# Performance work log

Measured on AMD Instinct MI355X. Metric: run time of the kernel, lower is better.

Reference implementation:

```python
import jax, jax.numpy as jnp
import numpy as np

B, N, D_MODEL, H, LIN_K = 4, 4096, 1024, 16, 256
D_K = D_MODEL // H


def setup_inputs() -> dict:
    key = jax.random.key(0)
    ks = jax.random.split(key, 9)
    s = 1.0 / np.sqrt(D_MODEL)
    return {
        "K": jax.random.normal(ks[0], (B, N, D_MODEL), jnp.float32),
        "Q": jax.random.normal(ks[1], (B, N, D_MODEL), jnp.float32),
        "V": jax.random.normal(ks[2], (B, N, D_MODEL), jnp.float32),
        "We": jax.random.normal(ks[3], (N, LIN_K), jnp.float32) / np.sqrt(N),
        "be": jnp.zeros((LIN_K,), jnp.float32),
        "Wf": jax.random.normal(ks[4], (N, LIN_K), jnp.float32) / np.sqrt(N),
        "bf": jnp.zeros((LIN_K,), jnp.float32),
        "Wo": jax.random.normal(ks[5], (D_MODEL, D_MODEL), jnp.float32) * s,
        "bo": jnp.zeros((D_MODEL,), jnp.float32),
        "n_heads": H,
    }


def reference(K, Q, V, We, be, Wf, bf, Wo, bo, n_heads):
    b, n, d_model = K.shape
    d_k = d_model // n_heads
    split = lambda x: x.reshape(b, n, n_heads, d_k).transpose(0, 2, 1, 3)  # [b,h,n,d]
    Kh, Qh, Vh = split(K), split(Q), split(V)
    # Linformer projection: Dense(k) applied to K^T [b,h,d,n] -> [b,h,d,k]
    Kp = jnp.einsum("bhnd,nk->bhdk", Kh, We) + be
    scores = jnp.einsum("bhnd,bhdk->bhnk", Qh, Kp) / jnp.sqrt(jnp.float32(d_k))
    P = jax.nn.softmax(scores, axis=-1)  # dropout rate 0.0 -> identity
    # V projection: Dense(k) on V^T then transpose back -> [b,h,k,d]
    Vp = jnp.einsum("bhnd,nk->bhkd", Vh, Wf) + bf[:, None]
    out = jnp.einsum("bhnk,bhkd->bhnd", P, Vp)
    out = out.transpose(0, 2, 1, 3).reshape(b, n, d_model)
    return out @ Wo + bo
```

## Files before the change

kernel.cpp:

```cpp
#include <hip/hip_runtime.h>
#include <hip/hip_bf16.h>

#define BB      4
#define SEQ     4096
#define DMODEL  1024
#define NHEAD   16
#define DK      64
#define LK      256
#define BH      (BB*NHEAD)

typedef unsigned short u16;
typedef unsigned int   u32;
typedef float f32x4  __attribute__((ext_vector_type(4)));
typedef _Float16 f16x8 __attribute__((ext_vector_type(8)));

__device__ __forceinline__ u16 f2h(float f) {
    _Float16 h = (_Float16)f;
    u16 r; __builtin_memcpy(&r, &h, 2); return r;
}
__device__ __forceinline__ u32 packh(float a, float b) {
    return (u32)f2h(a) | ((u32)f2h(b) << 16);
}
__device__ __forceinline__ void gl2lds16(const void* g, void* l) {
    __builtin_amdgcn_global_load_lds(
        (const __attribute__((address_space(1))) unsigned int*)g,
        (__attribute__((address_space(3))) unsigned int*)l,
        16, 0, 0);
}

__global__ __launch_bounds__(256) void tconv(
    const float* __restrict__ src, u16* __restrict__ dst,
    int ss, int ds, size_t sbo, size_t dbo)
{
    const float* S = src + (size_t)blockIdx.z * sbo;
    u16* D         = dst + (size_t)blockIdx.z * dbo;
    const int r0 = blockIdx.x * 64;
    const int c0 = blockIdx.y * 64;
    __shared__ float T[64][65];
    const int t = threadIdx.x;
    {
        int rr = (t >> 4) * 4;
        int cc = (t & 15) * 4;
#pragma unroll
        for (int i = 0; i < 4; ++i) {
            float4 v = *(const float4*)(S + (size_t)(r0 + rr + i) * ss + c0 + cc);
            T[rr + i][cc + 0] = v.x; T[rr + i][cc + 1] = v.y;
            T[rr + i][cc + 2] = v.z; T[rr + i][cc + 3] = v.w;
        }
    }
    __syncthreads();
    int cr = t >> 2, rc = (t & 3) * 16;
    u32 o[8];
#pragma unroll
    for (int j = 0; j < 8; ++j)
        o[j] = packh(T[rc + 2 * j][cr], T[rc + 2 * j + 1][cr]);
    u16* d = D + (size_t)(c0 + cr) * ds + r0 + rc;
    *(uint4*)(d)     = make_uint4(o[0], o[1], o[2], o[3]);
    *(uint4*)(d + 8) = make_uint4(o[4], o[5], o[6], o[7]);
}

__global__ __launch_bounds__(256) void wo_convert(
    const float* __restrict__ Wo, u16* __restrict__ WoT)
{
    const int n0 = blockIdx.x * 64, k0 = blockIdx.y * 64;
    __shared__ float T[64][65];
    const int t = threadIdx.x;
    {
        int kr = (t >> 4) * 4;
        int nc = (t & 15) * 4;
#pragma unroll
        for (int i = 0; i < 4; ++i) {
            float4 v = *(const float4*)(Wo + (size_t)(k0 + kr + i) * DMODEL + n0 + nc);
            T[kr + i][nc + 0] = v.x; T[kr + i][nc + 1] = v.y;
            T[kr + i][nc + 2] = v.z; T[kr + i][nc + 3] = v.w;
        }
    }
    __syncthreads();
    int n = t >> 2, kc = (t & 3) * 16;
    u32 o[8];
#pragma unroll
    for (int j = 0; j < 8; ++j)
        o[j] = packh(T[kc + j * 2][n], T[kc + j * 2 + 1][n]);
    u16* dst = WoT + (size_t)(n0 + n) * DMODEL + k0 + kc;
    *(uint4*)(dst)     = make_uint4(o[0], o[1], o[2], o[3]);
    *(uint4*)(dst + 8) = make_uint4(o[4], o[5], o[6], o[7]);
}

#define PROJ_BODY(Ab, Bb, bias, Cb, bias_on_row, c_row_stride, c0, r0)          \
    const int t  = threadIdx.x;                                                 \
    const int lane = t & 63;                                                    \
    const int w  = t >> 6;                                                      \
    const int wr = w >> 1, wc = w & 1;                                          \
    const int q  = lane >> 4, c = lane & 15;                                    \
    __shared__ u16 As[2][128 * 64];                                             \
    __shared__ u16 Bs[2][128 * 64];                                             \
    auto stage = [&](int buf, int kk) {                                         \
        _Pragma("unroll")                                                       \
        for (int i = 0; i < 4; ++i) {                                           \
            int li  = i * 256 + t;                                              \
            int row = li >> 3;                                                  \
            int c8  = (li & 7) ^ (row & 7);                                     \
            gl2lds16(Ab + (size_t)(r0 + row) * SEQ + kk + c8 * 8, &As[buf][(size_t)li * 8]); \
            gl2lds16(Bb + (size_t)(c0 + row) * SEQ + kk + c8 * 8, &Bs[buf][(size_t)li * 8]); \
        }                                                                       \
    };                                                                          \
    f32x4 acc[4][4];                                                            \
    _Pragma("unroll")                                                           \
    for (int m = 0; m < 4; ++m)                                                 \
        _Pragma("unroll")                                                       \
        for (int n = 0; n < 4; ++n) acc[m][n] = (f32x4){0.f, 0.f, 0.f, 0.f};    \
    stage(0, 0);                                                                \
    __syncthreads();                                                            \
    int cur = 0;                                                                \
    for (int k0 = 0; k0 < SEQ; k0 += 64) {                                      \
        if (k0 + 64 < SEQ) stage(cur ^ 1, k0 + 64);                             \
        _Pragma("unroll")                                                       \
        for (int s = 0; s < 2; ++s) {                                           \
            f16x8 af[4], bf[4];                                                 \
            _Pragma("unroll")                                                   \
            for (int m = 0; m < 4; ++m) {                                       \
                int row = wr * 64 + m * 16 + c;                                 \
                int c8  = (s * 4 + q) ^ (row & 7);                              \
                af[m] = *(const f16x8*)&As[cur][row * 64 + c8 * 8];             \
            }                                                                   \
            _Pragma("unroll")                                                   \
            for (int n = 0; n < 4; ++n) {                                       \
                int row = wc * 64 + n * 16 + c;                                 \
                int c8  = (s * 4 + q) ^ (row & 7);                              \
                bf[n] = *(const f16x8*)&Bs[cur][row * 64 + c8 * 8];             \
            }                                                                   \
            _Pragma("unroll")                                                   \
            for (int m = 0; m < 4; ++m)                                         \
                _Pragma("unroll")                                               \
                for (int n = 0; n < 4; ++n)                                     \
                    acc[m][n] = __builtin_amdgcn_mfma_f32_16x16x32_f16(af[m], bf[n], acc[m][n], 0, 0, 0); \
        }                                                                       \
        __syncthreads();                                                        \
        cur ^= 1;                                                               \
    }                                                                           \
    if (bias_on_row) {                                                          \
        _Pragma("unroll")                                                       \
        for (int m = 0; m < 4; ++m) {                                           \
            int rowb = r0 + wr * 64 + m * 16 + q * 4;                           \
            _Pragma("unroll")                                                   \
            for (int r = 0; r < 4; ++r) {                                       \
                float bv = bias[rowb + r];                                      \
                u16* dst = Cb + (size_t)(rowb + r) * c_row_stride + c0 + wc * 64 + c; \
                _Pragma("unroll")                                               \
                for (int n = 0; n < 4; ++n) dst[n * 16] = f2h(acc[m][n][r] + bv); \
            }                                                                   \
        }                                                                       \
    } else {                                                                    \
        float bv[4];                                                            \
        _Pragma("unroll")                                                       \
        for (int n = 0; n < 4; ++n) bv[n] = bias[c0 + wc * 64 + n * 16 + c];    \
        _Pragma("unroll")                                                       \
        for (int m = 0; m < 4; ++m) {                                           \
            int rowb = r0 + wr * 64 + m * 16 + q * 4;                           \
            _Pragma("unroll")                                                   \
            for (int r = 0; r < 4; ++r) {                                       \
                u16* dst = Cb + (size_t)(rowb + r) * c_row_stride + c0 + wc * 64 + c; \
                _Pragma("unroll")                                               \
                for (int n = 0; n < 4; ++n) dst[n * 16] = f2h(acc[m][n][r] + bv[n]); \
            }                                                                   \
        }                                                                       \
    }

__global__ __launch_bounds__(256) void proj_gemm(
    const u16* __restrict__ A, const u16* __restrict__ B,
    const float* __restrict__ bias, u16* __restrict__ Cout,
    int bias_on_row, size_t a_batch, size_t b_batch,
    int c_row_stride, size_t c_batch)
{
    const u16* Ab = A + (size_t)blockIdx.z * a_batch;
    const u16* Bb = B + (size_t)blockIdx.z * b_batch;
    u16* Cb       = Cout + (size_t)blockIdx.z * c_batch;
    const int c0 = blockIdx.x * 128;
    const int r0 = blockIdx.y * 128;
    PROJ_BODY(Ab, Bb, bias, Cb, bias_on_row, c_row_stride, c0, r0)
}

__global__ __launch_bounds__(256) void proj_both(
    const u16* __restrict__ WeT, const u16* __restrict__ WfT,
    const u16* __restrict__ KT,  const u16* __restrict__ VT,
    const float* __restrict__ be, const float* __restrict__ bfp,
    u16* __restrict__ KpF, u16* __restrict__ VpF)
{
    const int id = blockIdx.x;
    const u16 *Ab, *Bb; const float* bias; u16* Cb;
    int bias_on_row, c_row_stride, c0, r0;
    if (id < 64) {
        int b = id >> 4, s = id & 15;
        c0 = (s & 7) * 128; r0 = (s >> 3) * 128;
        Ab = WeT; Bb = KT + (size_t)b * DMODEL * SEQ;
        bias = be; bias_on_row = 1;
        Cb = KpF + (size_t)b * LK * DMODEL; c_row_stride = DMODEL;
    } else {
        int j = id - 64, b = j >> 4, s = j & 15;
        c0 = (s & 1) * 128; r0 = (s >> 1) * 128;
        Ab = VT + (size_t)b * DMODEL * SEQ; Bb = WfT;
        bias = bfp; bias_on_row = 0;
        Cb = VpF + (size_t)b * DMODEL * LK; c_row_stride = LK;
    }
    PROJ_BODY(Ab, Bb, bias, Cb, bias_on_row, c_row_stride, c0, r0)
}

__global__ __launch_bounds__(256) void attn_mfma(
    const float* __restrict__ Qin, const u16* __restrict__ KpF,
    const u16* __restrict__ VpF,   u16* __restrict__ AO)
{
    const int bh = blockIdx.y, b = bh >> 4, h = bh & 15;
    const int n0 = blockIdx.x * 64;
    const int t  = threadIdx.x;
    const int w    = t >> 6;
    const int lane = t & 63;
    const int q    = lane >> 4;
    const int c    = lane & 15;

    __shared__ u16 QO[64][72];
    __shared__ u16 KP[16896];
    __shared__ u16 Vl[16384];

    const u16* kbase = KpF + (size_t)b * LK * DMODEL + h * DK;
#pragma unroll
    for (int i = 0; i < 8; ++i) {
        int li = i * 256 + t;
        int row = li >> 3, ch = li & 7;
        int chs = ch ^ (row & 7);
        gl2lds16(kbase + (size_t)row * DMODEL + chs * 8, KP + (size_t)li * 8);
    }
    const u16* vbase = VpF + ((size_t)b * DMODEL + h * DK) * LK;
#pragma unroll
    for (int i = 0; i < 8; ++i) {
        int li = i * 256 + t;
        int row = li >> 5, ch = li & 31;
        int chs = (ch & 24) | ((ch & 7) ^ (row & 7));
        gl2lds16(vbase + (size_t)row * LK + chs * 8, Vl + (size_t)li * 8);
    }
    {
        int lr = lane >> 2, col0 = (lane & 3) * 16;
        const float* src = Qin + ((size_t)b * SEQ + n0 + w * 16 + lr) * DMODEL + h * DK + col0;
        float4 f0 = ((const float4*)src)[0];
        float4 f1 = ((const float4*)src)[1];
        float4 f2 = ((const float4*)src)[2];
        float4 f3 = ((const float4*)src)[3];
        uint4 p0, p1;
        p0.x = packh(f0.x, f0.y); p0.y = packh(f0.z, f0.w);
        p0.z = packh(f1.x, f1.y); p0.w = packh(f1.z, f1.w);
        p1.x = packh(f2.x, f2.y); p1.y = packh(f2.z, f2.w);
        p1.z = packh(f3.x, f3.y); p1.w = packh(f3.z, f3.w);
        *(uint4*)&QO[w * 16 + lr][col0]     = p0;
        *(uint4*)&QO[w * 16 + lr][col0 + 8] = p1;
    }
    __syncthreads();

    f16x8 a0 = *(const f16x8*)&QO[w * 16 + c][q * 8];
    f16x8 a1 = *(const f16x8*)&QO[w * 16 + c][32 + q * 8];

    f32x4 sc[16];
#pragma unroll
    for (int nt = 0; nt < 16; ++nt) sc[nt] = (f32x4){0.f, 0.f, 0.f, 0.f};
#pragma unroll
    for (int nt = 0; nt < 16; ++nt) {
        int ra = (nt * 16 + c) * 64;
        f16x8 b0 = *(const f16x8*)&KP[ra + ((q ^ (c & 7)) * 8)];
        f16x8 b1 = *(const f16x8*)&KP[ra + (((4 + q) ^ (c & 7)) * 8)];
        sc[nt] = __builtin_amdgcn_mfma_f32_16x16x32_f16(a0, b0, sc[nt], 0, 0, 0);
        sc[nt] = __builtin_amdgcn_mfma_f32_16x16x32_f16(a1, b1, sc[nt], 0, 0, 0);
    }

    float mx[4] = {-1e30f, -1e30f, -1e30f, -1e30f};
#pragma unroll
    for (int nt = 0; nt < 16; ++nt) {
        sc[nt] *= 0.125f;
#pragma unroll
        for (int r = 0; r < 4; ++r) mx[r] = fmaxf(mx[r], sc[nt][r]);
    }
#pragma unroll
    for (int d = 1; d < 16; d <<= 1)
#pragma unroll
        for (int r = 0; r < 4; ++r) mx[r] = fmaxf(mx[r], __shfl_xor(mx[r], d, 64));

    float sm[4] = {0.f, 0.f, 0.f, 0.f};
#pragma unroll
    for (int nt = 0; nt < 16; ++nt)
#pragma unroll
        for (int r = 0; r < 4; ++r) {
            float e = __expf(sc[nt][r] - mx[r]);
            sc[nt][r] = e;
            sm[r] += e;
        }
#pragma unroll
    for (int d = 1; d < 16; d <<= 1)
#pragma unroll
        for (int r = 0; r < 4; ++r) sm[r] += __shfl_xor(sm[r], d, 64);
    float inv[4];
#pragma unroll
    for (int r = 0; r < 4; ++r) inv[r] = 1.0f / sm[r];

    __syncthreads();

#pragma unroll
    for (int nt = 0; nt < 16; ++nt)
#pragma unroll
        for (int r = 0; r < 4; ++r)
            KP[(w * 16 + q * 4 + r) * 264 + nt * 16 + c] = f2h(sc[nt][r] * inv[r]);

    f32x4 ov[4];
#pragma unroll
    for (int nt = 0; nt < 4; ++nt) ov[nt] = (f32x4){0.f, 0.f, 0.f, 0.f};
#pragma unroll
    for (int ks = 0; ks < 8; ++ks) {
        f16x8 pa = *(const f16x8*)&KP[(w * 16 + c) * 264 + ks * 32 + q * 8];
#pragma unroll
        for (int nt = 0; nt < 4; ++nt) {
            int chunk = ks * 4 + q;
            int chs = (chunk & 24) | ((chunk & 7) ^ (c & 7));
            f16x8 vf = *(const f16x8*)&Vl[(nt * 16 + c) * 256 + chs * 8];
            ov[nt] = __builtin_amdgcn_mfma_f32_16x16x32_f16(pa, vf, ov[nt], 0, 0, 0);
        }
    }

#pragma unroll
    for (int nt = 0; nt < 4; ++nt)
#pragma unroll
        for (int r = 0; r < 4; ++r)
            QO[w * 16 + q * 4 + r][nt * 16 + c] = f2h(ov[nt][r]);

#pragma unroll
    for (int pass = 0; pass < 2; ++pass) {
        int lr  = w * 16 + pass * 8 + (lane >> 3);
        int col = (lane & 7) * 8;
        uint4 vv = *(uint4*)&QO[lr][col];
        *(uint4*)(AO + ((size_t)b * SEQ + n0 + lr) * DMODEL + h * DK + col) = vv;
    }
}

#define OBM 128
#define OBN 128
#define OBK 64

__global__ __launch_bounds__(256) void out_gemm_mfma(
    const u16* __restrict__ AO, const u16* __restrict__ WoT,
    const float* __restrict__ bo, float* __restrict__ Out)
{
    const int c0 = blockIdx.x * OBN;
    const int r0 = blockIdx.y * OBM;
    const int t  = threadIdx.x;
    const int lane = t & 63;
    const int w  = t >> 6;
    const int wr = w >> 1, wc = w & 1;
    const int q  = lane >> 4, c = lane & 15;

    __shared__ u16 As[OBM * OBK];
    __shared__ u16 Bs[OBN * OBK];

    f32x4 acc[4][4];
#pragma unroll
    for (int m = 0; m < 4; ++m)
#pragma unroll
        for (int n = 0; n < 4; ++n) acc[m][n] = (f32x4){0.f, 0.f, 0.f, 0.f};

    for (int k0 = 0; k0 < DMODEL; k0 += OBK) {
#pragma unroll
        for (int i = 0; i < 4; ++i) {
            int li  = i * 256 + t;
            int row = li >> 3;
            int c8  = (li & 7) ^ (row & 7);
            gl2lds16(AO  + (size_t)(r0 + row) * DMODEL + k0 + c8 * 8, (u16*)As + (size_t)li * 8);
            gl2lds16(WoT + (size_t)(c0 + row) * DMODEL + k0 + c8 * 8, (u16*)Bs + (size_t)li * 8);
        }
        __syncthreads();

#pragma unroll
        for (int s = 0; s < 2; ++s) {
            f16x8 af[4], bf[4];
#pragma unroll
            for (int m = 0; m < 4; ++m) {
                int row = wr * 64 + m * 16 + c;
                int c8  = (s * 4 + q) ^ (row & 7);
                af[m] = *(const f16x8*)&As[row * 64 + c8 * 8];
            }
#pragma unroll
            for (int n = 0; n < 4; ++n) {
                int row = wc * 64 + n * 16 + c;
                int c8  = (s * 4 + q) ^ (row & 7);
                bf[n] = *(const f16x8*)&Bs[row * 64 + c8 * 8];
            }
#pragma unroll
            for (int m = 0; m < 4; ++m)
#pragma unroll
                for (int n = 0; n < 4; ++n)
                    acc[m][n] = __builtin_amdgcn_mfma_f32_16x16x32_f16(af[m], bf[n], acc[m][n], 0, 0, 0);
        }
        __syncthreads();
    }

    float bv[4];
#pragma unroll
    for (int n = 0; n < 4; ++n) bv[n] = bo[c0 + wc * 64 + n * 16 + c];
#pragma unroll
    for (int m = 0; m < 4; ++m) {
        int rowb = r0 + wr * 64 + m * 16 + q * 4;
#pragma unroll
        for (int r = 0; r < 4; ++r) {
            float* dst = Out + (size_t)(rowb + r) * DMODEL + c0 + wc * 64 + c;
#pragma unroll
            for (int n = 0; n < 4; ++n) dst[n * 16] = acc[m][n][r] + bv[n];
        }
    }
}

extern "C" void kernel_launch(void* const* d_in, const int* in_sizes, int n_in,
                              void* d_out, int out_size, void* d_ws, size_t ws_size,
                              hipStream_t stream)
{
    const float* K   = (const float*)d_in[0];
    const float* Q   = (const float*)d_in[1];
    const float* V   = (const float*)d_in[2];
    const float* We  = (const float*)d_in[3];
    const float* be  = (const float*)d_in[4];
    const float* Wf  = (const float*)d_in[5];
    const float* bfp = (const float*)d_in[6];
    const float* Wo  = (const float*)d_in[7];
    const float* bo  = (const float*)d_in[8];
    float* Out = (float*)d_out;

    const size_t M1 = 1048576;
    const size_t TB = (size_t)BB * DMODEL * SEQ;

    if (ws_size >= 2 * (4 * M1 + 2 * TB)) {
        u16* KpF = (u16*)d_ws;
        u16* VpF = KpF + M1;
        u16* WeT = VpF + M1;
        u16* WfT = WeT + M1;
        u16* KT  = WfT + M1;
        u16* VT  = KT + TB;
        u16* AO  = KT;
        u16* WoT = WeT;

        tconv<<<dim3(SEQ / 64, LK / 64, 1), 256, 0, stream>>>(We, WeT, LK, SEQ, 0, 0);
        tconv<<<dim3(SEQ / 64, LK / 64, 1), 256, 0, stream>>>(Wf, WfT, LK, SEQ, 0, 0);
        tconv<<<dim3(SEQ / 64, DMODEL / 64, BB), 256, 0, stream>>>(
            K, KT, DMODEL, SEQ, (size_t)SEQ * DMODEL, (size_t)DMODEL * SEQ);
        tconv<<<dim3(SEQ / 64, DMODEL / 64, BB), 256, 0, stream>>>(
            V, VT, DMODEL, SEQ, (size_t)SEQ * DMODEL, (size_t)DMODEL * SEQ);
        proj_both<<<dim3(128), 256, 0, stream>>>(WeT, WfT, KT, VT, be, bfp, KpF, VpF);
        wo_convert<<<dim3(DMODEL / 64, DMODEL / 64), 256, 0, stream>>>(Wo, WoT);
        attn_mfma<<<dim3(SEQ / 64, BH), 256, 0, stream>>>(Q, KpF, VpF, AO);
        out_gemm_mfma<<<dim3(DMODEL / OBN, (BB * SEQ) / OBM), 256, 0, stream>>>(AO, WoT, bo, Out);
    } else {
        u16* KpF = (u16*)d_ws;
        u16* VpF = KpF + (size_t)BB * LK * DMODEL;
        u16* BIG = VpF + (size_t)BB * DMODEL * LK;
        u16* Wsm = BIG + (size_t)BB * SEQ * DMODEL;

        tconv<<<dim3(SEQ / 64, LK / 64, 1), 256, 0, stream>>>(We, Wsm, LK, SEQ, 0, 0);
        tconv<<<dim3(SEQ / 64, DMODEL / 64, BB), 256, 0, stream>>>(
            K, BIG, DMODEL, SEQ, (size_t)SEQ * DMODEL, (size_t)DMODEL * SEQ);
        proj_gemm<<<dim3(DMODEL / 128, LK / 128, BB), 256, 0, stream>>>(
            Wsm, BIG, be, KpF, 1, (size_t)0, (size_t)DMODEL * SEQ, DMODEL, (size_t)LK * DMODEL);
        tconv<<<dim3(SEQ / 64, LK / 64, 1), 256, 0, stream>>>(Wf, Wsm, LK, SEQ, 0, 0);
        tconv<<<dim3(SEQ / 64, DMODEL / 64, BB), 256, 0, stream>>>(
            V, BIG, DMODEL, SEQ, (size_t)SEQ * DMODEL, (size_t)DMODEL * SEQ);
        proj_gemm<<<dim3(LK / 128, DMODEL / 128, BB), 256, 0, stream>>>(
            BIG, Wsm, bfp, VpF, 0, (size_t)DMODEL * SEQ, (size_t)0, LK, (size_t)DMODEL * LK);
        wo_convert<<<dim3(DMODEL / 64, DMODEL / 64), 256, 0, stream>>>(Wo, Wsm);
        attn_mfma<<<dim3(SEQ / 64, BH), 256, 0, stream>>>(Q, KpF, VpF, BIG);
        out_gemm_mfma<<<dim3(DMODEL / OBN, (BB * SEQ) / OBM), 256, 0, stream>>>(BIG, Wsm, bo, Out);
    }
}
```

Before: 395.5 us.

## Make attention blocks persistent over 1024 rows to reuse projected K/V tiles

The attention kernel now uses 512-thread blocks that each handle 1024 query rows in 8 passes of 128. The projected K and V tiles for a head are loaded into LDS once per block instead of once per 64 rows. Q is read straight from global memory into registers and prefetched one pass ahead, with no LDS staging. The grid shrinks to 256 blocks, which lowers parallelism and latency hiding. The softmax probabilities and the output staging share one per-wave LDS region, relying on each wave's rows being private.

```diff
diff --git a/kernel.cpp b/kernel.cpp
--- a/kernel.cpp
+++ b/kernel.cpp
@@ -20,6 +20,12 @@
 }
 __device__ __forceinline__ u32 packh(float a, float b) {
     return (u32)f2h(a) | ((u32)f2h(b) << 16);
+}
+__device__ __forceinline__ f16x8 pack8h(float4 a, float4 b) {
+    union { uint4 u; f16x8 h; } r;
+    r.u = make_uint4(packh(a.x, a.y), packh(a.z, a.w),
+                     packh(b.x, b.y), packh(b.z, b.w));
+    return r.h;
 }
 __device__ __forceinline__ void gl2lds16(const void* g, void* l) {
     __builtin_amdgcn_global_load_lds(
@@ -205,134 +211,129 @@
     PROJ_BODY(Ab, Bb, bias, Cb, bias_on_row, c_row_stride, c0, r0)
 }
 
-__global__ __launch_bounds__(256) void attn_mfma(
+__global__ __launch_bounds__(512) void attn_mfma(
     const float* __restrict__ Qin, const u16* __restrict__ KpF,
     const u16* __restrict__ VpF,   u16* __restrict__ AO)
 {
     const int bh = blockIdx.y, b = bh >> 4, h = bh & 15;
-    const int n0 = blockIdx.x * 64;
+    const int n0 = blockIdx.x * 1024;
     const int t  = threadIdx.x;
     const int w    = t >> 6;
     const int lane = t & 63;
     const int q    = lane >> 4;
     const int c    = lane & 15;
 
-    __shared__ u16 QO[64][72];
-    __shared__ u16 KP[16896];
+    __shared__ u16 Kl[16384];
     __shared__ u16 Vl[16384];
+    __shared__ u16 Pl[128 * 264];
 
     const u16* kbase = KpF + (size_t)b * LK * DMODEL + h * DK;
 #pragma unroll
-    for (int i = 0; i < 8; ++i) {
-        int li = i * 256 + t;
+    for (int i = 0; i < 4; ++i) {
+        int li = i * 512 + t;
         int row = li >> 3, ch = li & 7;
         int chs = ch ^ (row & 7);
-        gl2lds16(kbase + (size_t)row * DMODEL + chs * 8, KP + (size_t)li * 8);
+        gl2lds16(kbase + (size_t)row * DMODEL + chs * 8, Kl + (size_t)li * 8);
     }
     const u16* vbase = VpF + ((size_t)b * DMODEL + h * DK) * LK;
 #pragma unroll
-    for (int i = 0; i < 8; ++i) {
-        int li = i * 256 + t;
+    for (int i = 0; i < 4; ++i) {
+        int li = i * 512 + t;
         int row = li >> 5, ch = li & 31;
         int chs = (ch & 24) | ((ch & 7) ^ (row & 7));
         gl2lds16(vbase + (size_t)row * LK + chs * 8, Vl + (size_t)li * 8);
     }
-    {
-        int lr = lane >> 2, col0 = (lane & 3) * 16;
-        const float* src = Qin + ((size_t)b * SEQ + n0 + w * 16 + lr) * DMODEL + h * DK + col0;
-        float4 f0 = ((const float4*)src)[0];
-        float4 f1 = ((const float4*)src)[1];
-        float4 f2 = ((const float4*)src)[2];
-        float4 f3 = ((const float4*)src)[3];
-        uint4 p0, p1;
-        p0.x = packh(f0.x, f0.y); p0.y = packh(f0.z, f0.w);
-        p0.z = packh(f1.x, f1.y); p0.w = packh(f1.z, f1.w);
-        p1.x = packh(f2.x, f2.y); p1.y = packh(f2.z, f2.w);
-        p1.z = packh(f3.x, f3.y); p1.w = packh(f3.z, f3.w);
-        *(uint4*)&QO[w * 16 + lr][col0]     = p0;
-        *(uint4*)&QO[w * 16 + lr][col0 + 8] = p1;
-    }
     __syncthreads();
 
-    f16x8 a0 = *(const f16x8*)&QO[w * 16 + c][q * 8];
-    f16x8 a1 = *(const f16x8*)&QO[w * 16 + c][32 + q * 8];
-
-    f32x4 sc[16];
-#pragma unroll
-    for (int nt = 0; nt < 16; ++nt) sc[nt] = (f32x4){0.f, 0.f, 0.f, 0.f};
-#pragma unroll
-    for (int nt = 0; nt < 16; ++nt) {
-        int ra = (nt * 16 + c) * 64;
-        f16x8 b0 = *(const f16x8*)&KP[ra + ((q ^ (c & 7)) * 8)];
-        f16x8 b1 = *(const f16x8*)&KP[ra + (((4 + q) ^ (c & 7)) * 8)];
-        sc[nt] = __builtin_amdgcn_mfma_f32_16x16x32_f16(a0, b0, sc[nt], 0, 0, 0);
-        sc[nt] = __builtin_amdgcn_mfma_f32_16x16x32_f16(a1, b1, sc[nt], 0, 0, 0);
-    }
-
-    float mx[4] = {-1e30f, -1e30f, -1e30f, -1e30f};
-#pragma unroll
-    for (int nt = 0; nt < 16; ++nt) {
-        sc[nt] *= 0.125f;
-#pragma unroll
-        for (int r = 0; r < 4; ++r) mx[r] = fmaxf(mx[r], sc[nt][r]);
-    }
-#pragma unroll
-    for (int d = 1; d < 16; d <<= 1)
-#pragma unroll
-        for (int r = 0; r < 4; ++r) mx[r] = fmaxf(mx[r], __shfl_xor(mx[r], d, 64));
-
-    float sm[4] = {0.f, 0.f, 0.f, 0.f};
-#pragma unroll
-    for (int nt = 0; nt < 16; ++nt)
-#pragma unroll
-        for (int r = 0; r < 4; ++r) {
-            float e = __expf(sc[nt][r] - mx[r]);
-            sc[nt][r] = e;
-            sm[r] += e;
-        }
-#pragma unroll
-    for (int d = 1; d < 16; d <<= 1)
-#pragma unroll
-        for (int r = 0; r < 4; ++r) sm[r] += __shfl_xor(sm[r], d, 64);
-    float inv[4];
-#pragma unroll
-    for (int r = 0; r < 4; ++r) inv[r] = 1.0f / sm[r];
-
-    __syncthreads();
-
-#pragma unroll
-    for (int nt = 0; nt < 16; ++nt)
-#pragma unroll
-        for (int r = 0; r < 4; ++r)
-            KP[(w * 16 + q * 4 + r) * 264 + nt * 16 + c] = f2h(sc[nt][r] * inv[r]);
-
-    f32x4 ov[4];
-#pragma unroll
-    for (int nt = 0; nt < 4; ++nt) ov[nt] = (f32x4){0.f, 0.f, 0.f, 0.f};
-#pragma unroll
-    for (int ks = 0; ks < 8; ++ks) {
-        f16x8 pa = *(const f16x8*)&KP[(w * 16 + c) * 264 + ks * 32 + q * 8];
-#pragma unroll
-        for (int nt = 0; nt < 4; ++nt) {
-            int chunk = ks * 4 + q;
-            int chs = (chunk & 24) | ((chunk & 7) ^ (c & 7));
-            f16x8 vf = *(const f16x8*)&Vl[(nt * 16 + c) * 256 + chs * 8];
-            ov[nt] = __builtin_amdgcn_mfma_f32_16x16x32_f16(pa, vf, ov[nt], 0, 0, 0);
-        }
-    }
-
-#pragma unroll
-    for (int nt = 0; nt < 4; ++nt)
-#pragma unroll
-        for (int r = 0; r < 4; ++r)
-            QO[w * 16 + q * 4 + r][nt * 16 + c] = f2h(ov[nt][r]);
-
-#pragma unroll
-    for (int pass = 0; pass < 2; ++pass) {
-        int lr  = w * 16 + pass * 8 + (lane >> 3);
-        int col = (lane & 7) * 8;
-        uint4 vv = *(uint4*)&QO[lr][col];
-        *(uint4*)(AO + ((size_t)b * SEQ + n0 + lr) * DMODEL + h * DK + col) = vv;
+    const float* qbase = Qin + ((size_t)b * SEQ + n0 + w * 16 + c) * DMODEL + h * DK;
+    const float4* qp0 = (const float4*)qbase;
+    float4 q0 = qp0[2 * q], q1 = qp0[2 * q + 1];
+    float4 q2 = qp0[8 + 2 * q], q3 = qp0[8 + 2 * q + 1];
+
+    for (int p = 0; p < 8; ++p) {
+        f16x8 a0 = pack8h(q0, q1);
+        f16x8 a1 = pack8h(q2, q3);
+        if (p < 7) {
+            const float4* qp = (const float4*)(qbase + (size_t)(p + 1) * 128 * DMODEL);
+            q0 = qp[2 * q]; q1 = qp[2 * q + 1];
+            q2 = qp[8 + 2 * q]; q3 = qp[8 + 2 * q + 1];
+        }
+
+        f32x4 sc[16];
+#pragma unroll
+        for (int nt = 0; nt < 16; ++nt) sc[nt] = (f32x4){0.f, 0.f, 0.f, 0.f};
+#pragma unroll
+        for (int nt = 0; nt < 16; ++nt) {
+            int ra = (nt * 16 + c) * 64;
+            f16x8 b0 = *(const f16x8*)&Kl[ra + ((q ^ (c & 7)) * 8)];
+            f16x8 b1 = *(const f16x8*)&Kl[ra + (((4 + q) ^ (c & 7)) * 8)];
+            sc[nt] = __builtin_amdgcn_mfma_f32_16x16x32_f16(a0, b0, sc[nt], 0, 0, 0);
+            sc[nt] = __builtin_amdgcn_mfma_f32_16x16x32_f16(a1, b1, sc[nt], 0, 0, 0);
+        }
+
+        float mx[4] = {-1e30f, -1e30f, -1e30f, -1e30f};
+#pragma unroll
+        for (int nt = 0; nt < 16; ++nt) {
+            sc[nt] *= 0.125f;
+#pragma unroll
+            for (int r = 0; r < 4; ++r) mx[r] = fmaxf(mx[r], sc[nt][r]);
+        }
+#pragma unroll
+        for (int d = 1; d < 16; d <<= 1)
+#pragma unroll
+            for (int r = 0; r < 4; ++r) mx[r] = fmaxf(mx[r], __shfl_xor(mx[r], d, 64));
+
+        float sm[4] = {0.f, 0.f, 0.f, 0.f};
+#pragma unroll
+        for (int nt = 0; nt < 16; ++nt)
+#pragma unroll
+            for (int r = 0; r < 4; ++r) {
+                float e = __expf(sc[nt][r] - mx[r]);
+                sc[nt][r] = e;
+                sm[r] += e;
+            }
+#pragma unroll
+        for (int d = 1; d < 16; d <<= 1)
+#pragma unroll
+            for (int r = 0; r < 4; ++r) sm[r] += __shfl_xor(sm[r], d, 64);
+        float inv[4];
+#pragma unroll
+        for (int r = 0; r < 4; ++r) inv[r] = 1.0f / sm[r];
+
+#pragma unroll
+        for (int nt = 0; nt < 16; ++nt)
+#pragma unroll
+            for (int r = 0; r < 4; ++r)
+                Pl[(w * 16 + q * 4 + r) * 264 + nt * 16 + c] = f2h(sc[nt][r] * inv[r]);
+
+        f32x4 ov[4];
+#pragma unroll
+        for (int nt = 0; nt < 4; ++nt) ov[nt] = (f32x4){0.f, 0.f, 0.f, 0.f};
+#pragma unroll
+        for (int ks = 0; ks < 8; ++ks) {
+            f16x8 pa = *(const f16x8*)&Pl[(w * 16 + c) * 264 + ks * 32 + q * 8];
+#pragma unroll
+            for (int nt = 0; nt < 4; ++nt) {
+                int chunk = ks * 4 + q;
+                int chs = (chunk & 24) | ((chunk & 7) ^ (c & 7));
+                f16x8 vf = *(const f16x8*)&Vl[(nt * 16 + c) * 256 + chs * 8];
+                ov[nt] = __builtin_amdgcn_mfma_f32_16x16x32_f16(pa, vf, ov[nt], 0, 0, 0);
+            }
+        }
+
+#pragma unroll
+        for (int nt = 0; nt < 4; ++nt)
+#pragma unroll
+            for (int r = 0; r < 4; ++r)
+                Pl[(w * 16 + q * 4 + r) * 264 + nt * 16 + c] = f2h(ov[nt][r]);
+
+#pragma unroll
+        for (int ps = 0; ps < 2; ++ps) {
+            int lr  = w * 16 + ps * 8 + (lane >> 3);
+            int col = (lane & 7) * 8;
+            uint4 vv = *(uint4*)&Pl[lr * 264 + col];
+            *(uint4*)(AO + ((size_t)b * SEQ + n0 + p * 128 + lr) * DMODEL + h * DK + col) = vv;
+        }
     }
 }
 
@@ -447,7 +448,7 @@
             V, VT, DMODEL, SEQ, (size_t)SEQ * DMODEL, (size_t)DMODEL * SEQ);
         proj_both<<<dim3(128), 256, 0, stream>>>(WeT, WfT, KT, VT, be, bfp, KpF, VpF);
         wo_convert<<<dim3(DMODEL / 64, DMODEL / 64), 256, 0, stream>>>(Wo, WoT);
-        attn_mfma<<<dim3(SEQ / 64, BH), 256, 0, stream>>>(Q, KpF, VpF, AO);
+        attn_mfma<<<dim3(4, BH), 512, 0, stream>>>(Q, KpF, VpF, AO);
         out_gemm_mfma<<<dim3(DMODEL / OBN, (BB * SEQ) / OBM), 256, 0, stream>>>(AO, WoT, bo, Out);
     } else {
         u16* KpF = (u16*)d_ws;
@@ -466,7 +467,7 @@
         proj_gemm<<<dim3(LK / 128, DMODEL / 128, BB), 256, 0, stream>>>(
             BIG, Wsm, bfp, VpF, 0, (size_t)DMODEL * SEQ, (size_t)0, LK, (size_t)DMODEL * LK);
         wo_convert<<<dim3(DMODEL / 64, DMODEL / 64), 256, 0, stream>>>(Wo, Wsm);
-        attn_mfma<<<dim3(SEQ / 64, BH), 256, 0, stream>>>(Q, KpF, VpF, BIG);
+        attn_mfma<<<dim3(4, BH), 512, 0, stream>>>(Q, KpF, VpF, BIG);
         out_gemm_mfma<<<dim3(DMODEL / OBN, (BB * SEQ) / OBM), 256, 0, stream>>>(BIG, Wsm, bo, Out);
     }
 }
```

After: 379.6 us. -4.0%, faster.
